# Kernel optimization log

Measured on AMD Instinct MI355X. Metric: run time of the kernel, lower is better.

## Reference

```python
import jax, jax.numpy as jnp
import numpy as np

NUM_CLASSES = 10
CLS_W, L1_W, GIOU_W = 2.0, 5.0, 2.0


def box_cxcywh_to_xyxy(b):
    cx, cy, w, h = b[..., 0], b[..., 1], b[..., 2], b[..., 3]
    return jnp.stack([cx - w / 2, cy - h / 2, cx + w / 2, cy + h / 2], axis=-1)


def giou_matrix(b1, b2):
    # b1: (B,N,4), b2: (B,M,4) xyxy -> (B,N,M)
    a1 = jnp.clip(b1[..., 2] - b1[..., 0], 0) * jnp.clip(b1[..., 3] - b1[..., 1], 0)
    a2 = jnp.clip(b2[..., 2] - b2[..., 0], 0) * jnp.clip(b2[..., 3] - b2[..., 1], 0)
    lt = jnp.maximum(b1[..., :, None, :2], b2[..., None, :, :2])
    rb = jnp.minimum(b1[..., :, None, 2:], b2[..., None, :, 2:])
    wh = jnp.clip(rb - lt, 0)
    inter = wh[..., 0] * wh[..., 1]
    union = a1[..., :, None] + a2[..., None, :] - inter
    iou = inter / jnp.clip(union, 1e-6)
    lte = jnp.minimum(b1[..., :, None, :2], b2[..., None, :, :2])
    rbe = jnp.maximum(b1[..., :, None, 2:], b2[..., None, :, 2:])
    whe = jnp.clip(rbe - lte, 0)
    enc = whe[..., 0] * whe[..., 1]
    return iou - (enc - union) / jnp.clip(enc, 1e-6)


def giou_elem(b1, b2):
    # b1, b2: (N,4) xyxy, paired -> (N,)
    a1 = jnp.clip(b1[:, 2] - b1[:, 0], 0) * jnp.clip(b1[:, 3] - b1[:, 1], 0)
    a2 = jnp.clip(b2[:, 2] - b2[:, 0], 0) * jnp.clip(b2[:, 3] - b2[:, 1], 0)
    lt = jnp.maximum(b1[:, :2], b2[:, :2])
    rb = jnp.minimum(b1[:, 2:], b2[:, 2:])
    wh = jnp.clip(rb - lt, 0)
    inter = wh[:, 0] * wh[:, 1]
    union = a1 + a2 - inter
    iou = inter / jnp.clip(union, 1e-6)
    lte = jnp.minimum(b1[:, :2], b2[:, :2])
    rbe = jnp.maximum(b1[:, 2:], b2[:, 2:])
    whe = jnp.clip(rbe - lte, 0)
    enc = whe[:, 0] * whe[:, 1]
    return iou - (enc - union) / jnp.clip(enc, 1e-6)


def hungarian(cost):
    # Jonker-Volgenant style shortest-augmenting-path assignment (== scipy.linear_sum_assignment)
    cost = np.asarray(cost, dtype=np.float64)
    transposed = cost.shape[0] > cost.shape[1]
    C = cost.T if transposed else cost
    n, m = C.shape  # n <= m
    u = np.zeros(n + 1)
    v = np.zeros(m + 1)
    p = np.zeros(m + 1, dtype=np.int64)
    colr = np.arange(m + 1)
    for i in range(1, n + 1):
        p[0] = i
        j0 = 0
        minv = np.full(m + 1, np.inf)
        way = np.zeros(m + 1, dtype=np.int64)
        used = np.zeros(m + 1, dtype=bool)
        while True:
            used[j0] = True
            i0 = p[j0]
            unused = colr[1:][~used[1:]]
            cur = C[i0 - 1, unused - 1] - u[i0] - v[unused]
            better = cur < minv[unused]
            bidx = unused[better]
            minv[bidx] = cur[better]
            way[bidx] = j0
            j1 = unused[np.argmin(minv[unused])]
            delta = minv[j1]
            u[p[used]] += delta
            v[used] -= delta
            minv[~used] -= delta
            j0 = j1
            if p[j0] == 0:
                break
        while j0 != 0:
            jn = way[j0]
            p[j0] = p[jn]
            j0 = jn
    rows = p[1:] - 1
    cols = np.arange(m)
    sel = rows >= 0
    r, c = rows[sel], cols[sel]
    if transposed:
        r, c = c, r
    order = np.argsort(r)
    return r[order], c[order]


def compute_matches(pred_logits, pred_boxes, gt_classes, gt_boxes):
    # Batched cost matrices on device, per-sample Hungarian on host (mirrors torch.no_grad matcher).
    B, Q, _ = pred_logits.shape
    G = gt_classes.shape[1]
    prob = jax.nn.softmax(pred_logits, axis=-1)
    cls_idx = jnp.clip(gt_classes, 0, NUM_CLASSES - 1)
    idx = jnp.broadcast_to(cls_idx[:, None, :], (B, Q, G))
    cls_cost = -jnp.take_along_axis(prob, idx, axis=2)                 # (B,Q,G)
    l1_cost = jnp.abs(pred_boxes[:, :, None, :] - gt_boxes[:, None, :, :]).sum(-1)
    g = giou_matrix(box_cxcywh_to_xyxy(pred_boxes), box_cxcywh_to_xyxy(gt_boxes))
    cost = CLS_W * cls_cost + L1_W * l1_cost - GIOU_W * g
    cost_np = np.asarray(jax.device_get(cost))
    valid_np = np.asarray(jax.device_get(gt_classes)) >= 0
    bs, ps, gs = [], [], []
    for bi in range(B):
        vidx = np.nonzero(valid_np[bi])[0]
        if vidx.size == 0:
            continue
        r, c = hungarian(cost_np[bi][:, vidx])
        bs.append(np.full(r.size, bi, dtype=np.int64))
        ps.append(r.astype(np.int64))
        gs.append(vidx[c].astype(np.int64))
    if bs:
        return np.concatenate(bs), np.concatenate(ps), np.concatenate(gs)
    z = np.zeros(0, np.int64)
    return z, z, z


def detection_loss(pred_logits, pred_boxes, gt_boxes, target_cls, b_f, p_f, g_f, n_matched):
    C1 = pred_logits.shape[-1]
    logp = jax.nn.log_softmax(pred_logits, axis=-1).reshape(-1, C1)
    t = target_cls.reshape(-1)
    w = jnp.ones(C1, dtype=pred_logits.dtype).at[-1].set(0.1)
    nll = -jnp.take_along_axis(logp, t[:, None], axis=1)[:, 0]
    wt = w[t]
    cls_loss = (wt * nll).sum() / wt.sum()
    mp = pred_boxes[b_f, p_f]
    mg = gt_boxes[b_f, g_f]
    l1 = jnp.abs(mp - mg).sum()
    gd = giou_elem(box_cxcywh_to_xyxy(mp), box_cxcywh_to_xyxy(mg))
    gl = (1.0 - gd).sum()
    return CLS_W * cls_loss + L1_W * l1 / n_matched + GIOU_W * gl / n_matched


def setup_inputs() -> dict:
    key = jax.random.key(0)
    k1, k2, k3, k4, k5 = jax.random.split(key, 5)
    B, Q, G, C = 64, 900, 100, NUM_CLASSES
    pred_logits = jax.random.normal(k1, (B, Q, C + 1), dtype=jnp.float32)
    pred_boxes = jax.random.uniform(k2, (B, Q, 4), dtype=jnp.float32, minval=0.05, maxval=0.6)
    gt_boxes = jax.random.uniform(k3, (B, G, 4), dtype=jnp.float32, minval=0.05, maxval=0.6)
    cls = jax.random.randint(k4, (B, G), 0, C)
    nvalid = jax.random.randint(k5, (B,), 1, G + 1)
    mask = jnp.arange(G)[None, :] < nvalid[:, None]
    gt_classes = jnp.where(mask, cls, -1).astype(jnp.int32)
    return {"pred_logits": pred_logits, "pred_boxes": pred_boxes,
            "gt_classes": gt_classes, "gt_boxes": gt_boxes}


def reference(pred_logits, pred_boxes, gt_classes, gt_boxes):
    B, Q = pred_logits.shape[:2]
    b_f, p_f, g_f = compute_matches(pred_logits, pred_boxes, gt_classes, gt_boxes)
    gt_np = np.asarray(jax.device_get(gt_classes))
    tc = np.full((B, Q), NUM_CLASSES, dtype=np.int32)
    tc[b_f, p_f] = gt_np[b_f, g_f]
    n_matched = max(int(b_f.size), 1)
    return detection_loss(pred_logits, pred_boxes, gt_boxes, jnp.asarray(tc), b_f, p_f, g_f, n_matched)
```

## Files before the change

### kernel.cpp

```cpp
#include <hip/hip_runtime.h>
#include <hip/hip_bf16.h>
#include <math.h>

#define BB 64
#define QQ 900
#define GG 100
#define NCLS 10
#define CP1 11

#define STRIDE 960
#define KPL 15
#define NT 512
#define NW 8
#define QMASK 255
#define ROUND_CAP 20000

#define NCH 8
#define QCH 128

#define CLS_W 2.0f
#define L1_W 5.0f
#define GIOU_W 2.0f

struct Accum {
  double wnll, wt, l1, gl;
  int nm, counter;
  int pad[6];
};

__global__ __launch_bounds__(256) void cost_kernel(
    const float* __restrict__ logits, const float* __restrict__ pboxes,
    const int* __restrict__ gcls, const float* __restrict__ gboxes,
    float* __restrict__ cost, float4* __restrict__ part, Accum* acc) {
  const int b = blockIdx.y;
  const int chunk = blockIdx.x;
  const int tid = threadIdx.x;
  const int ql = tid & (QCH - 1);
  const int gh = tid >> 7;
  const int q = chunk * QCH + ql;

  if (chunk == 0 && b == 0 && tid == 0) {
    acc->wnll = 0.0; acc->wt = 0.0; acc->l1 = 0.0; acc->gl = 0.0;
    acc->nm = 0; acc->counter = 0;
  }

  __shared__ float s_gb[GG * 4];
  __shared__ int   s_gc[GG];
  __shared__ float s_prob[QCH * 13];
  __shared__ float s_c[GG][QCH + 1];
  __shared__ float pm1[2][GG], pm2[2][GG];
  __shared__ int   pj1[2][GG];
  __shared__ int   sh_n;

  if (tid == 0) sh_n = 0;
  __syncthreads();

  for (int i = tid; i < GG * 4; i += 256) s_gb[i] = gboxes[b * GG * 4 + i];
  for (int i = tid; i < GG; i += 256) {
    const int v = gcls[b * GG + i];
    s_gc[i] = v;
    if (v >= 0) atomicAdd(&sh_n, 1);
  }

  float pcx = 0.f, pcy = 0.f, pw = 0.f, ph = 0.f;
  if (q < QQ) {
    const float* pb = pboxes + ((size_t)b * QQ + q) * 4;
    pcx = pb[0]; pcy = pb[1]; pw = pb[2]; ph = pb[3];
    if (gh == 0) {
      const float* lg = logits + ((size_t)b * QQ + q) * CP1;
      float l[CP1];
      float mx = -1e30f;
      for (int c = 0; c < CP1; ++c) { l[c] = lg[c]; mx = fmaxf(mx, l[c]); }
      float se = 0.f;
      for (int c = 0; c < CP1; ++c) { l[c] = expf(l[c] - mx); se += l[c]; }
      const float inv = 1.0f / se;
      for (int c = 0; c < NCLS; ++c) s_prob[ql * 13 + c] = l[c] * inv;
    }
  }
  __syncthreads();
  const int sn = sh_n;

  const float px1 = pcx - 0.5f * pw, py1 = pcy - 0.5f * ph;
  const float px2 = pcx + 0.5f * pw, py2 = pcy + 0.5f * ph;
  const float pa = fmaxf(px2 - px1, 0.f) * fmaxf(py2 - py1, 0.f);

  float* crow = cost + ((size_t)b * GG) * STRIDE + q;
  for (int g = gh; g < sn; g += 2) {
    float cv = 3e38f;
    if (q < QQ) {
      int cls = s_gc[g];
      cls = cls < 0 ? 0 : (cls > NCLS - 1 ? NCLS - 1 : cls);
      const float cc = -s_prob[ql * 13 + cls];
      const float gcx = s_gb[g * 4 + 0], gcy = s_gb[g * 4 + 1];
      const float gw  = s_gb[g * 4 + 2], gh2 = s_gb[g * 4 + 3];
      const float l1 = fabsf(pcx - gcx) + fabsf(pcy - gcy) + fabsf(pw - gw) + fabsf(ph - gh2);
      const float gx1 = gcx - 0.5f * gw, gy1 = gcy - 0.5f * gh2;
      const float gx2 = gcx + 0.5f * gw, gy2 = gcy + 0.5f * gh2;
      const float ga = fmaxf(gx2 - gx1, 0.f) * fmaxf(gy2 - gy1, 0.f);
      const float ltx = fmaxf(px1, gx1), lty = fmaxf(py1, gy1);
      const float rbx = fminf(px2, gx2), rby = fminf(py2, gy2);
      const float iw = fmaxf(rbx - ltx, 0.f), ih = fmaxf(rby - lty, 0.f);
      const float inter = iw * ih;
      const float uni = pa + ga - inter;
      const float iou = inter / fmaxf(uni, 1e-6f);
      const float ex1 = fminf(px1, gx1), ey1 = fminf(py1, gy1);
      const float ex2 = fmaxf(px2, gx2), ey2 = fmaxf(py2, gy2);
      const float ew = fmaxf(ex2 - ex1, 0.f), eh = fmaxf(ey2 - ey1, 0.f);
      const float enc = ew * eh;
      const float giou = iou - (enc - uni) / fmaxf(enc, 1e-6f);
      cv = CLS_W * cc + L1_W * l1 - GIOU_W * giou;
      crow[(size_t)g * STRIDE] = cv;
    } else if (q < STRIDE) {
      crow[(size_t)g * STRIDE] = 1e30f;
    }
    s_c[g][ql] = cv;
  }
  __syncthreads();

  {
    const int kmax = (chunk == NCH - 1) ? (QQ - (NCH - 1) * QCH) : QCH;
    const int half = tid >> 7;
    const int r = tid & 127;
    if (r < sn) {
      const int k0 = half ? 64 : 0;
      const int k1 = half ? kmax : (kmax < 64 ? kmax : 64);
      float m1 = 3e38f, m2 = 3e38f;
      int j1 = 0x7FFFFFFF;
      for (int k = k0; k < k1; ++k) {
        const float c = s_c[r][k];
        if (c < m1) { m2 = m1; m1 = c; j1 = 1 + chunk * QCH + k; }
        else if (c < m2) m2 = c;
      }
      pm1[half][r] = m1; pm2[half][r] = m2; pj1[half][r] = j1;
    }
    __syncthreads();
    if (tid < sn) {
      float m1 = pm1[0][tid], m2 = pm2[0][tid];
      int j1 = pj1[0][tid];
      const float n1 = pm1[1][tid], n2 = pm2[1][tid];
      const int i1 = pj1[1][tid];
      if (n1 < m1) { m2 = fminf(m1, n2); m1 = n1; j1 = i1; }
      else m2 = fminf(m2, n1);
      part[((size_t)b * NCH + chunk) * QCH + tid] = make_float4(m1, m2, __int_as_float(j1), 0.f);
    }
  }
}

__global__ __launch_bounds__(NT) void jv_kernel(
    const float* __restrict__ logits, const float* __restrict__ pboxes,
    const int* __restrict__ gcls, const float* __restrict__ gboxes,
    const float* __restrict__ cost, const float4* __restrict__ part,
    Accum* acc, float* out) {
  const int b = blockIdx.x;
  const int tid = threadIdx.x;
  const int lane = tid & 63;
  const int w = tid >> 6;

  __shared__ float vl[STRIDE + 2];
  __shared__ int   p[QQ + 1];
  __shared__ unsigned long long way64[STRIDE + 2];
  __shared__ float m1l[GG + 1], m2l[GG + 1];
  __shared__ int   aminl[GG + 1];
  __shared__ int   s_gc[GG];
  __shared__ int   queue[QMASK + 1];
  __shared__ int   sh_n, sh_qtail, sh_head;
  __shared__ double r0[NW], r1[NW], r2[NW], r3[NW];
  __shared__ int r4[NW];
  __shared__ float s_lse[QQ], s_mx[QQ];
  __shared__ float cbuf[NW][STRIDE];
  __shared__ int   ctag[NW];

  if (tid == 0) { sh_n = 0; sh_qtail = 0; sh_head = 0; }
  if (tid < NW) ctag[tid] = 0;
  for (int j = tid; j <= QQ; j += NT) p[j] = 0;
  for (int j = tid; j < STRIDE + 2; j += NT) { vl[j] = 0.f; way64[j] = 0ull; }
  if (tid < GG) s_gc[tid] = gcls[b * GG + tid];
  __syncthreads();
  if (tid < GG && s_gc[tid] >= 0) atomicAdd(&sh_n, 1);
  __syncthreads();
  const int n = sh_n;
  const float* Cb = cost + (size_t)b * GG * STRIDE;

  for (int r = tid; r < n; r += NT) {
    float m1 = 3e38f, m2 = 3e38f;
    int j1 = 0x7FFFFFFF;
#pragma unroll
    for (int ch = 0; ch < NCH; ++ch) {
      const float4 pr = part[((size_t)b * NCH + ch) * QCH + r];
      const float pm1 = pr.x, pm2 = pr.y;
      if (pm1 < m1) { m2 = fminf(m1, pm2); m1 = pm1; j1 = __float_as_int(pr.z); }
      else m2 = fminf(m2, pm1);
    }
    m1l[r] = m1; m2l[r] = m2; aminl[r] = j1;
  }
  for (int qq = tid; qq < QQ; qq += NT) {
    const float* lg = logits + ((size_t)b * QQ + qq) * CP1;
    float l[CP1];
    float mx = -1e30f;
    for (int c = 0; c < CP1; ++c) { l[c] = lg[c]; mx = fmaxf(mx, l[c]); }
    float se = 0.f;
    for (int c = 0; c < CP1; ++c) se += expf(l[c] - mx);
    s_mx[qq] = mx;
    s_lse[qq] = logf(se);
  }
  __syncthreads();

  if (tid < n) {
    const float regret = m2l[tid] - m1l[tid];
    const unsigned long long key =
        ((unsigned long long)__float_as_uint(regret) << 20) | (unsigned long long)(tid + 1);
    atomicMax(&way64[aminl[tid]], key);
  }
  __syncthreads();
  if (tid < n) {
    const int j1 = aminl[tid];
    if ((int)(way64[j1] & 0xFFFFFu) == tid + 1) {
      p[j1] = tid + 1;
      vl[j1] = m1l[tid] - m2l[tid];
    } else {
      const int t0 = atomicAdd(&sh_qtail, 1);
      queue[t0 & QMASK] = tid + 1;
    }
  }
  __syncthreads();
  for (int j = tid; j < STRIDE + 2; j += NT) way64[j] = 0ull;
  __syncthreads();

  {
    float pfA[KPL], pfB[KPL];
    int pfApos = -1, pfBpos = -1, pfArid = 0, pfBrid = 0;
    int kround = 0;
    while (kround < ROUND_CAP) {
      const int head = sh_head, tail = sh_qtail;
      const int nq = tail - head;
      if (nq <= 0) break;
      const int take = nq < 2 * NW ? nq : 2 * NW;
      ++kround;

      if (take <= NW) {
        const bool doA = (w < take);
        int ridA = 0;
        float m1A = 3e38f, m2A = 3e38f;
        int j1A = 0x7FFFFFFF;
        int k0A = 0;
        float sfA[KPL];
        if (doA) {
          const int posA = head + w;
          float rcA[KPL];
          if (pfApos == posA) {
            ridA = pfArid;
#pragma unroll
            for (int k = 0; k < KPL; ++k) rcA[k] = pfA[k];
          } else {
            ridA = queue[posA & QMASK];
            const unsigned long long hit =
                __ballot((lane < NW) && (ctag[lane] == ridA));
            if (hit) {
              const int slot = __ffsll((long long)hit) - 1;
#pragma unroll
              for (int k = 0; k < KPL; ++k) rcA[k] = cbuf[slot][lane + (k << 6)];
            } else {
              const float* Cr = Cb + (size_t)(ridA - 1) * STRIDE + lane;
#pragma unroll
              for (int k = 0; k < KPL; ++k) rcA[k] = Cr[k << 6];
            }
          }
          float nA1 = 3e38f, nA2 = 3e38f;
          int iA1 = 0x7FFFFFFF;
#pragma unroll
          for (int k = 0; k < 8; ++k) {
            const float cA = rcA[k] - vl[1 + lane + (k << 6)];
            if (cA < m1A) { m2A = m1A; m1A = cA; j1A = 1 + lane + (k << 6); }
            else if (cA < m2A) m2A = cA;
          }
#pragma unroll
          for (int k = 8; k < KPL; ++k) {
            const float cA = rcA[k] - vl[1 + lane + (k << 6)];
            if (cA < nA1) { nA2 = nA1; nA1 = cA; iA1 = 1 + lane + (k << 6); }
            else if (cA < nA2) nA2 = cA;
          }
          if (nA1 < m1A) { m2A = fminf(m1A, nA2); m1A = nA1; j1A = iA1; }
          else m2A = fminf(m2A, nA1);
          for (int m = 1; m < 64; m <<= 1) {
            const float oA1 = __shfl_xor(m1A, m), oA2 = __shfl_xor(m2A, m);
            const int ojA = __shfl_xor(j1A, m);
            if (oA1 < m1A) { m2A = fminf(m1A, oA2); m1A = oA1; j1A = ojA; }
            else m2A = fminf(m2A, oA1);
          }
          k0A = p[j1A];
          if (k0A > 0) {
            const float* Cr = Cb + (size_t)(k0A - 1) * STRIDE + lane;
#pragma unroll
            for (int k = 0; k < KPL; ++k) sfA[k] = Cr[k << 6];
          }
          if (lane == 0) {
            float dA = m2A - m1A;
            if (dA < 0.f) dA = 0.f;
            const unsigned long long keyA = ((unsigned long long)kround << 44) |
                ((unsigned long long)__float_as_uint(dA) << 12) | (unsigned long long)ridA;
            atomicMax(&way64[j1A], keyA);
          }
        }
        pfApos = -1; pfBpos = -1;
        {
          const int nh = head + take;
          const int pA = nh + w;
          if (pA < tail) {
            pfArid = queue[pA & QMASK];
            const float* Cr = Cb + (size_t)(pfArid - 1) * STRIDE + lane;
#pragma unroll
            for (int k = 0; k < KPL; ++k) pfA[k] = Cr[k << 6];
            pfApos = pA;
          }
        }
        __syncthreads();
        if (doA && k0A > 0) {
#pragma unroll
          for (int k = 0; k < KPL; ++k) cbuf[w][lane + (k << 6)] = sfA[k];
          if (lane == 0) ctag[w] = k0A;
        }
        if (lane == 0 && doA) {
          if ((int)(way64[j1A] & 0xFFFu) == ridA) {
            float dA = m2A - m1A;
            if (dA < 0.f) dA = 0.f;
            const float ov = vl[j1A];
            float nv = ov - dA;
            if (!(nv < ov)) nv = nextafterf(ov, -3e38f);
            vl[j1A] = nv;
            const int k0 = p[j1A];
            p[j1A] = ridA;
            if (k0 > 0) { const int t0 = atomicAdd(&sh_qtail, 1); queue[t0 & QMASK] = k0; }
          } else {
            const int t0 = atomicAdd(&sh_qtail, 1);
            queue[t0 & QMASK] = ridA;
          }
        }
        if (tid == 0) sh_head = head + take;
        __syncthreads();
      } else {
        const bool doA = (w < take);
        const bool doB = (NW + w < take);
        int ridA = 0, ridB = 0;
        float m1A = 3e38f, m2A = 3e38f, m1B = 3e38f, m2B = 3e38f;
        int j1A = 0x7FFFFFFF, j1B = 0x7FFFFFFF;
        {
          float rcA[KPL], rcB[KPL];
          const int posA = head + w;
          if (pfApos == posA) {
            ridA = pfArid;
#pragma unroll
            for (int k = 0; k < KPL; ++k) rcA[k] = pfA[k];
          } else {
            ridA = queue[posA & QMASK];
            const float* Cr = Cb + (size_t)(ridA - 1) * STRIDE + lane;
#pragma unroll
            for (int k = 0; k < KPL; ++k) rcA[k] = Cr[k << 6];
          }
          if (doB) {
            const int posB = head + NW + w;
            if (pfBpos == posB) {
              ridB = pfBrid;
#pragma unroll
              for (int k = 0; k < KPL; ++k) rcB[k] = pfB[k];
            } else {
              ridB = queue[posB & QMASK];
              const float* Cr = Cb + (size_t)(ridB - 1) * STRIDE + lane;
#pragma unroll
              for (int k = 0; k < KPL; ++k) rcB[k] = Cr[k << 6];
            }
          } else {
#pragma unroll
            for (int k = 0; k < KPL; ++k) rcB[k] = 3e38f;
          }
          float nA1 = 3e38f, nA2 = 3e38f, nB1 = 3e38f, nB2 = 3e38f;
          int iA1 = 0x7FFFFFFF, iB1 = 0x7FFFFFFF;
#pragma unroll
          for (int k = 0; k < 8; ++k) {
            const float vv = vl[1 + lane + (k << 6)];
            const float cA = rcA[k] - vv;
            if (cA < m1A) { m2A = m1A; m1A = cA; j1A = 1 + lane + (k << 6); }
            else if (cA < m2A) m2A = cA;
            const float cB = rcB[k] - vv;
            if (cB < m1B) { m2B = m1B; m1B = cB; j1B = 1 + lane + (k << 6); }
            else if (cB < m2B) m2B = cB;
          }
#pragma unroll
          for (int k = 8; k < KPL; ++k) {
            const float vv = vl[1 + lane + (k << 6)];
            const float cA = rcA[k] - vv;
            if (cA < nA1) { nA2 = nA1; nA1 = cA; iA1 = 1 + lane + (k << 6); }
            else if (cA < nA2) nA2 = cA;
            const float cB = rcB[k] - vv;
            if (cB < nB1) { nB2 = nB1; nB1 = cB; iB1 = 1 + lane + (k << 6); }
            else if (cB < nB2) nB2 = cB;
          }
          if (nA1 < m1A) { m2A = fminf(m1A, nA2); m1A = nA1; j1A = iA1; }
          else m2A = fminf(m2A, nA1);
          if (nB1 < m1B) { m2B = fminf(m1B, nB2); m1B = nB1; j1B = iB1; }
          else m2B = fminf(m2B, nB1);
          for (int m = 1; m < 64; m <<= 1) {
            const float oA1 = __shfl_xor(m1A, m), oA2 = __shfl_xor(m2A, m);
            const int ojA = __shfl_xor(j1A, m);
            const float oB1 = __shfl_xor(m1B, m), oB2 = __shfl_xor(m2B, m);
            const int ojB = __shfl_xor(j1B, m);
            if (oA1 < m1A) { m2A = fminf(m1A, oA2); m1A = oA1; j1A = ojA; }
            else m2A = fminf(m2A, oA1);
            if (oB1 < m1B) { m2B = fminf(m1B, oB2); m1B = oB1; j1B = ojB; }
            else m2B = fminf(m2B, oB1);
          }
          if (lane == 0) {
            float dA = m2A - m1A;
            if (dA < 0.f) dA = 0.f;
            const unsigned long long keyA = ((unsigned long long)kround << 44) |
                ((unsigned long long)__float_as_uint(dA) << 12) | (unsigned long long)ridA;
            atomicMax(&way64[j1A], keyA);
            if (doB) {
              float dB = m2B - m1B;
              if (dB < 0.f) dB = 0.f;
              const unsigned long long keyB = ((unsigned long long)kround << 44) |
                  ((unsigned long long)__float_as_uint(dB) << 12) | (unsigned long long)ridB;
              atomicMax(&way64[j1B], keyB);
            }
          }
        }
        pfApos = -1; pfBpos = -1;
        {
          const int nh = head + take;
          const int pA = nh + w, pB = nh + NW + w;
          if (pA < tail) {
            pfArid = queue[pA & QMASK];
            const float* Cr = Cb + (size_t)(pfArid - 1) * STRIDE + lane;
#pragma unroll
            for (int k = 0; k < KPL; ++k) pfA[k] = Cr[k << 6];
            pfApos = pA;
          }
          if (pB < tail) {
            pfBrid = queue[pB & QMASK];
            const float* Cr = Cb + (size_t)(pfBrid - 1) * STRIDE + lane;
#pragma unroll
            for (int k = 0; k < KPL; ++k) pfB[k] = Cr[k << 6];
            pfBpos = pB;
          }
        }
        __syncthreads();
        if (lane == 0 && doA) {
          if ((int)(way64[j1A] & 0xFFFu) == ridA) {
            float dA = m2A - m1A;
            if (dA < 0.f) dA = 0.f;
            const float ov = vl[j1A];
            float nv = ov - dA;
            if (!(nv < ov)) nv = nextafterf(ov, -3e38f);
            vl[j1A] = nv;
            const int k0 = p[j1A];
            p[j1A] = ridA;
            if (k0 > 0) { const int t0 = atomicAdd(&sh_qtail, 1); queue[t0 & QMASK] = k0; }
          } else {
            const int t0 = atomicAdd(&sh_qtail, 1);
            queue[t0 & QMASK] = ridA;
          }
          if (doB) {
            if ((int)(way64[j1B] & 0xFFFu) == ridB) {
              float dB = m2B - m1B;
              if (dB < 0.f) dB = 0.f;
              const float ov = vl[j1B];
              float nv = ov - dB;
              if (!(nv < ov)) nv = nextafterf(ov, -3e38f);
              vl[j1B] = nv;
              const int k0 = p[j1B];
              p[j1B] = ridB;
              if (k0 > 0) { const int t0 = atomicAdd(&sh_qtail, 1); queue[t0 & QMASK] = k0; }
            } else {
              const int t0 = atomicAdd(&sh_qtail, 1);
              queue[t0 & QMASK] = ridB;
            }
          }
        }
        if (tid == 0) sh_head = head + take;
        __syncthreads();
      }
    }
  }
  __syncthreads();

  double wnll = 0.0, wt = 0.0, l1d = 0.0, gld = 0.0;
  int nm = 0;
  for (int q = tid; q < QQ; q += NT) {
    const int idx = b * QQ + q;
    const int g = p[q + 1] - 1;
    const int t = (g >= 0) ? s_gc[g] : NCLS;
    const float lt = logits[(size_t)idx * CP1 + t];
    const float logp = (lt - s_mx[q]) - s_lse[q];
    const float wgt = (t == NCLS) ? 0.1f : 1.0f;
    wnll += (double)(wgt * (-logp));
    wt += (double)wgt;
    if (g >= 0) {
      nm += 1;
      const float* pb = pboxes + (size_t)idx * 4;
      const float* gb = gboxes + ((size_t)b * GG + g) * 4;
      const float pcx = pb[0], pcy = pb[1], pw = pb[2], ph = pb[3];
      const float gcx = gb[0], gcy = gb[1], gw = gb[2], gh = gb[3];
      const float l1 = fabsf(pcx - gcx) + fabsf(pcy - gcy) + fabsf(pw - gw) + fabsf(ph - gh);
      const float px1 = pcx - 0.5f * pw, py1 = pcy - 0.5f * ph;
      const float px2 = pcx + 0.5f * pw, py2 = pcy + 0.5f * ph;
      const float gx1 = gcx - 0.5f * gw, gy1 = gcy - 0.5f * gh;
      const float gx2 = gcx + 0.5f * gw, gy2 = gcy + 0.5f * gh;
      const float pa = fmaxf(px2 - px1, 0.f) * fmaxf(py2 - py1, 0.f);
      const float ga = fmaxf(gx2 - gx1, 0.f) * fmaxf(gy2 - gy1, 0.f);
      const float ltx = fmaxf(px1, gx1), lty = fmaxf(py1, gy1);
      const float rbx = fminf(px2, gx2), rby = fminf(py2, gy2);
      const float iw = fmaxf(rbx - ltx, 0.f), ih = fmaxf(rby - lty, 0.f);
      const float inter = iw * ih;
      const float uni = pa + ga - inter;
      const float iou = inter / fmaxf(uni, 1e-6f);
      const float ex1 = fminf(px1, gx1), ey1 = fminf(py1, gy1);
      const float ex2 = fmaxf(px2, gx2), ey2 = fmaxf(py2, gy2);
      const float ew = fmaxf(ex2 - ex1, 0.f), eh = fmaxf(ey2 - ey1, 0.f);
      const float enc = ew * eh;
      const float giou = iou - (enc - uni) / fmaxf(enc, 1e-6f);
      l1d += (double)l1;
      gld += (double)(1.0f - giou);
    }
  }

  for (int off = 32; off; off >>= 1) {
    wnll += __shfl_down(wnll, off);
    wt   += __shfl_down(wt, off);
    l1d  += __shfl_down(l1d, off);
    gld  += __shfl_down(gld, off);
    nm   += __shfl_down(nm, off);
  }
  if (lane == 0) { r0[w] = wnll; r1[w] = wt; r2[w] = l1d; r3[w] = gld; r4[w] = nm; }
  __syncthreads();
  if (tid == 0) {
    for (int x = 1; x < NW; ++x) { wnll += r0[x]; wt += r1[x]; l1d += r2[x]; gld += r3[x]; nm += r4[x]; }
    atomicAdd(&acc->wnll, wnll);
    atomicAdd(&acc->wt, wt);
    atomicAdd(&acc->l1, l1d);
    atomicAdd(&acc->gl, gld);
    atomicAdd(&acc->nm, nm);
    __threadfence();
    const int ticket = atomicAdd(&acc->counter, 1);
    if (ticket == BB - 1) {
      const double fw = atomicAdd(&acc->wnll, 0.0);
      const double fwt = atomicAdd(&acc->wt, 0.0);
      const double fl1 = atomicAdd(&acc->l1, 0.0);
      const double fgl = atomicAdd(&acc->gl, 0.0);
      int fnm = atomicAdd(&acc->nm, 0);
      if (fnm < 1) fnm = 1;
      const double loss = (double)CLS_W * (fw / fwt) +
                          ((double)L1_W * fl1 + (double)GIOU_W * fgl) / (double)fnm;
      out[0] = (float)loss;
    }
  }
}

extern "C" void kernel_launch(void* const* d_in, const int* in_sizes, int n_in,
                              void* d_out, int out_size, void* d_ws, size_t ws_size,
                              hipStream_t stream) {
  const float* logits = (const float*)d_in[0];
  const float* pboxes = (const float*)d_in[1];
  const int*   gcls   = (const int*)d_in[2];
  const float* gboxes = (const float*)d_in[3];

  char* ws = (char*)d_ws;
  Accum* acc = (Accum*)ws;
  float4* part = (float4*)(ws + 4096);
  float* cost = (float*)(ws + 4096 + (size_t)BB * NCH * QCH * sizeof(float4));

  cost_kernel<<<dim3(NCH, BB), 256, 0, stream>>>(logits, pboxes, gcls, gboxes, cost, part, acc);
  jv_kernel<<<BB, NT, 0, stream>>>(logits, pboxes, gcls, gboxes, cost, part, acc, (float*)d_out);
}
```

Baseline: 102.8 us.

## Fuse cost-matrix kernel into JV assignment kernel with shared-memory scratch reuse

Removes the separate cost_kernel and computes the cost matrix inside the per-batch JV kernel. Each wavefront computes one GT row, writes it to global memory and reduces the row min, second-min and argmin with shuffles, replacing the per-chunk partial results. Prediction boxes, probabilities and areas are staged in shared memory and aliased over the cbuf scratch. The accumulator is zeroed with a memset. This saves a launch and the partial-min round-trip, but cost computation now runs on only 64 blocks instead of 512, which lowers parallelism for that phase.

```diff
diff --git a/kernel.cpp b/kernel.cpp
--- a/kernel.cpp
+++ b/kernel.cpp
@@ -1,5 +1,4 @@
 #include <hip/hip_runtime.h>
-#include <hip/hip_bf16.h>
 #include <math.h>
 
 #define BB 64
@@ -15,12 +14,11 @@
 #define QMASK 255
 #define ROUND_CAP 20000
 
-#define NCH 8
-#define QCH 128
-
 #define CLS_W 2.0f
 #define L1_W 5.0f
 #define GIOU_W 2.0f
+
+#define SCRATCH_F 13504
 
 struct Accum {
   double wnll, wt, l1, gl;
@@ -28,181 +26,129 @@
   int pad[6];
 };
 
-__global__ __launch_bounds__(256) void cost_kernel(
+__global__ __launch_bounds__(NT) void det_kernel(
     const float* __restrict__ logits, const float* __restrict__ pboxes,
     const int* __restrict__ gcls, const float* __restrict__ gboxes,
-    float* __restrict__ cost, float4* __restrict__ part, Accum* acc) {
-  const int b = blockIdx.y;
-  const int chunk = blockIdx.x;
-  const int tid = threadIdx.x;
-  const int ql = tid & (QCH - 1);
-  const int gh = tid >> 7;
-  const int q = chunk * QCH + ql;
-
-  if (chunk == 0 && b == 0 && tid == 0) {
-    acc->wnll = 0.0; acc->wt = 0.0; acc->l1 = 0.0; acc->gl = 0.0;
-    acc->nm = 0; acc->counter = 0;
-  }
-
-  __shared__ float s_gb[GG * 4];
-  __shared__ int   s_gc[GG];
-  __shared__ float s_prob[QCH * 13];
-  __shared__ float s_c[GG][QCH + 1];
-  __shared__ float pm1[2][GG], pm2[2][GG];
-  __shared__ int   pj1[2][GG];
-  __shared__ int   sh_n;
-
-  if (tid == 0) sh_n = 0;
-  __syncthreads();
-
-  for (int i = tid; i < GG * 4; i += 256) s_gb[i] = gboxes[b * GG * 4 + i];
-  for (int i = tid; i < GG; i += 256) {
-    const int v = gcls[b * GG + i];
-    s_gc[i] = v;
-    if (v >= 0) atomicAdd(&sh_n, 1);
-  }
-
-  float pcx = 0.f, pcy = 0.f, pw = 0.f, ph = 0.f;
-  if (q < QQ) {
-    const float* pb = pboxes + ((size_t)b * QQ + q) * 4;
-    pcx = pb[0]; pcy = pb[1]; pw = pb[2]; ph = pb[3];
-    if (gh == 0) {
-      const float* lg = logits + ((size_t)b * QQ + q) * CP1;
-      float l[CP1];
-      float mx = -1e30f;
-      for (int c = 0; c < CP1; ++c) { l[c] = lg[c]; mx = fmaxf(mx, l[c]); }
-      float se = 0.f;
-      for (int c = 0; c < CP1; ++c) { l[c] = expf(l[c] - mx); se += l[c]; }
-      const float inv = 1.0f / se;
-      for (int c = 0; c < NCLS; ++c) s_prob[ql * 13 + c] = l[c] * inv;
-    }
-  }
-  __syncthreads();
-  const int sn = sh_n;
-
-  const float px1 = pcx - 0.5f * pw, py1 = pcy - 0.5f * ph;
-  const float px2 = pcx + 0.5f * pw, py2 = pcy + 0.5f * ph;
-  const float pa = fmaxf(px2 - px1, 0.f) * fmaxf(py2 - py1, 0.f);
-
-  float* crow = cost + ((size_t)b * GG) * STRIDE + q;
-  for (int g = gh; g < sn; g += 2) {
-    float cv = 3e38f;
-    if (q < QQ) {
-      int cls = s_gc[g];
-      cls = cls < 0 ? 0 : (cls > NCLS - 1 ? NCLS - 1 : cls);
-      const float cc = -s_prob[ql * 13 + cls];
-      const float gcx = s_gb[g * 4 + 0], gcy = s_gb[g * 4 + 1];
-      const float gw  = s_gb[g * 4 + 2], gh2 = s_gb[g * 4 + 3];
-      const float l1 = fabsf(pcx - gcx) + fabsf(pcy - gcy) + fabsf(pw - gw) + fabsf(ph - gh2);
-      const float gx1 = gcx - 0.5f * gw, gy1 = gcy - 0.5f * gh2;
-      const float gx2 = gcx + 0.5f * gw, gy2 = gcy + 0.5f * gh2;
-      const float ga = fmaxf(gx2 - gx1, 0.f) * fmaxf(gy2 - gy1, 0.f);
-      const float ltx = fmaxf(px1, gx1), lty = fmaxf(py1, gy1);
-      const float rbx = fminf(px2, gx2), rby = fminf(py2, gy2);
-      const float iw = fmaxf(rbx - ltx, 0.f), ih = fmaxf(rby - lty, 0.f);
-      const float inter = iw * ih;
-      const float uni = pa + ga - inter;
-      const float iou = inter / fmaxf(uni, 1e-6f);
-      const float ex1 = fminf(px1, gx1), ey1 = fminf(py1, gy1);
-      const float ex2 = fmaxf(px2, gx2), ey2 = fmaxf(py2, gy2);
-      const float ew = fmaxf(ex2 - ex1, 0.f), eh = fmaxf(ey2 - ey1, 0.f);
-      const float enc = ew * eh;
-      const float giou = iou - (enc - uni) / fmaxf(enc, 1e-6f);
-      cv = CLS_W * cc + L1_W * l1 - GIOU_W * giou;
-      crow[(size_t)g * STRIDE] = cv;
-    } else if (q < STRIDE) {
-      crow[(size_t)g * STRIDE] = 1e30f;
-    }
-    s_c[g][ql] = cv;
-  }
-  __syncthreads();
-
-  {
-    const int kmax = (chunk == NCH - 1) ? (QQ - (NCH - 1) * QCH) : QCH;
-    const int half = tid >> 7;
-    const int r = tid & 127;
-    if (r < sn) {
-      const int k0 = half ? 64 : 0;
-      const int k1 = half ? kmax : (kmax < 64 ? kmax : 64);
-      float m1 = 3e38f, m2 = 3e38f;
-      int j1 = 0x7FFFFFFF;
-      for (int k = k0; k < k1; ++k) {
-        const float c = s_c[r][k];
-        if (c < m1) { m2 = m1; m1 = c; j1 = 1 + chunk * QCH + k; }
-        else if (c < m2) m2 = c;
-      }
-      pm1[half][r] = m1; pm2[half][r] = m2; pj1[half][r] = j1;
-    }
-    __syncthreads();
-    if (tid < sn) {
-      float m1 = pm1[0][tid], m2 = pm2[0][tid];
-      int j1 = pj1[0][tid];
-      const float n1 = pm1[1][tid], n2 = pm2[1][tid];
-      const int i1 = pj1[1][tid];
-      if (n1 < m1) { m2 = fminf(m1, n2); m1 = n1; j1 = i1; }
-      else m2 = fminf(m2, n1);
-      part[((size_t)b * NCH + chunk) * QCH + tid] = make_float4(m1, m2, __int_as_float(j1), 0.f);
-    }
-  }
-}
-
-__global__ __launch_bounds__(NT) void jv_kernel(
-    const float* __restrict__ logits, const float* __restrict__ pboxes,
-    const int* __restrict__ gcls, const float* __restrict__ gboxes,
-    const float* __restrict__ cost, const float4* __restrict__ part,
-    Accum* acc, float* out) {
+    float* __restrict__ cost, Accum* acc, float* out) {
   const int b = blockIdx.x;
   const int tid = threadIdx.x;
   const int lane = tid & 63;
   const int w = tid >> 6;
 
-  __shared__ float vl[STRIDE + 2];
-  __shared__ int   p[QQ + 1];
+  __shared__ float4 s_pb4[QQ];
+  __shared__ float  s_gb[GG * 4];
+  __shared__ int    s_gc[GG];
+  __shared__ float  s_mx[QQ], s_lse[QQ];
+  __shared__ float  vl[STRIDE + 2];
+  __shared__ int    p[QQ + 1];
   __shared__ unsigned long long way64[STRIDE + 2];
-  __shared__ float m1l[GG + 1], m2l[GG + 1];
-  __shared__ int   aminl[GG + 1];
-  __shared__ int   s_gc[GG];
-  __shared__ int   queue[QMASK + 1];
-  __shared__ int   sh_n, sh_qtail, sh_head;
+  __shared__ float  m1l[GG], m2l[GG];
+  __shared__ int    aminl[GG];
+  __shared__ int    queue[QMASK + 1];
+  __shared__ int    sh_n, sh_qtail, sh_head;
   __shared__ double r0[NW], r1[NW], r2[NW], r3[NW];
-  __shared__ int r4[NW];
-  __shared__ float s_lse[QQ], s_mx[QQ];
-  __shared__ float cbuf[NW][STRIDE];
-  __shared__ int   ctag[NW];
+  __shared__ int    r4[NW];
+  __shared__ int    ctag[NW];
+  __shared__ float4 scratch4[SCRATCH_F / 4];
+
+  float* scratch = (float*)scratch4;
+  float*  s_prob = scratch;
+  float4* s_pxy  = (float4*)(scratch + 9004);
+  float*  s_pa   = scratch + 9004 + 3600;
 
   if (tid == 0) { sh_n = 0; sh_qtail = 0; sh_head = 0; }
   if (tid < NW) ctag[tid] = 0;
   for (int j = tid; j <= QQ; j += NT) p[j] = 0;
   for (int j = tid; j < STRIDE + 2; j += NT) { vl[j] = 0.f; way64[j] = 0ull; }
+  for (int i = tid; i < GG * 4; i += NT) s_gb[i] = gboxes[b * GG * 4 + i];
   if (tid < GG) s_gc[tid] = gcls[b * GG + tid];
-  __syncthreads();
-  if (tid < GG && s_gc[tid] >= 0) atomicAdd(&sh_n, 1);
-  __syncthreads();
-  const int n = sh_n;
-  const float* Cb = cost + (size_t)b * GG * STRIDE;
-
-  for (int r = tid; r < n; r += NT) {
-    float m1 = 3e38f, m2 = 3e38f;
-    int j1 = 0x7FFFFFFF;
-#pragma unroll
-    for (int ch = 0; ch < NCH; ++ch) {
-      const float4 pr = part[((size_t)b * NCH + ch) * QCH + r];
-      const float pm1 = pr.x, pm2 = pr.y;
-      if (pm1 < m1) { m2 = fminf(m1, pm2); m1 = pm1; j1 = __float_as_int(pr.z); }
-      else m2 = fminf(m2, pm1);
-    }
-    m1l[r] = m1; m2l[r] = m2; aminl[r] = j1;
-  }
   for (int qq = tid; qq < QQ; qq += NT) {
+    const float4 pb = reinterpret_cast<const float4*>(pboxes)[(size_t)b * QQ + qq];
+    s_pb4[qq] = pb;
+    const float px1 = pb.x - 0.5f * pb.z, py1 = pb.y - 0.5f * pb.w;
+    const float px2 = pb.x + 0.5f * pb.z, py2 = pb.y + 0.5f * pb.w;
+    s_pxy[qq] = make_float4(px1, py1, px2, py2);
+    s_pa[qq] = fmaxf(px2 - px1, 0.f) * fmaxf(py2 - py1, 0.f);
     const float* lg = logits + ((size_t)b * QQ + qq) * CP1;
     float l[CP1];
     float mx = -1e30f;
     for (int c = 0; c < CP1; ++c) { l[c] = lg[c]; mx = fmaxf(mx, l[c]); }
     float se = 0.f;
-    for (int c = 0; c < CP1; ++c) se += expf(l[c] - mx);
+    for (int c = 0; c < CP1; ++c) { l[c] = expf(l[c] - mx); se += l[c]; }
+    const float inv = 1.0f / se;
+    for (int c = 0; c < NCLS; ++c) s_prob[qq * NCLS + c] = l[c] * inv;
     s_mx[qq] = mx;
     s_lse[qq] = logf(se);
   }
+  __syncthreads();
+  if (tid < GG && s_gc[tid] >= 0) atomicAdd(&sh_n, 1);
+  __syncthreads();
+  const int n = sh_n;
+  float* Cb = cost + (size_t)b * GG * STRIDE;
+
+  auto cell = [&](int qv, int cls, float gcx, float gcy, float gwv, float ghv,
+                  float gx1, float gy1, float gx2, float gy2, float ga) -> float {
+    const float cc = -s_prob[qv * NCLS + cls];
+    const float4 pb = s_pb4[qv];
+    const float4 pxy = s_pxy[qv];
+    const float pa = s_pa[qv];
+    const float l1v = fabsf(pb.x - gcx) + fabsf(pb.y - gcy) +
+                      fabsf(pb.z - gwv) + fabsf(pb.w - ghv);
+    const float ltx = fmaxf(pxy.x, gx1), lty = fmaxf(pxy.y, gy1);
+    const float rbx = fminf(pxy.z, gx2), rby = fminf(pxy.w, gy2);
+    const float iw = fmaxf(rbx - ltx, 0.f), ih = fmaxf(rby - lty, 0.f);
+    const float inter = iw * ih;
+    const float uni = pa + ga - inter;
+    const float iou = inter / fmaxf(uni, 1e-6f);
+    const float ex1 = fminf(pxy.x, gx1), ey1 = fminf(pxy.y, gy1);
+    const float ex2 = fmaxf(pxy.z, gx2), ey2 = fmaxf(pxy.w, gy2);
+    const float ew = fmaxf(ex2 - ex1, 0.f), eh = fmaxf(ey2 - ey1, 0.f);
+    const float enc = ew * eh;
+    const float giou = iou - (enc - uni) / fmaxf(enc, 1e-6f);
+    return CLS_W * cc + L1_W * l1v - GIOU_W * giou;
+  };
+
+  for (int r = w; r < n; r += NW) {
+    int cls = s_gc[r];
+    cls = cls < 0 ? 0 : (cls > NCLS - 1 ? NCLS - 1 : cls);
+    const float gcx = s_gb[r * 4 + 0], gcy = s_gb[r * 4 + 1];
+    const float gwv = s_gb[r * 4 + 2], ghv = s_gb[r * 4 + 3];
+    const float gx1 = gcx - 0.5f * gwv, gy1 = gcy - 0.5f * ghv;
+    const float gx2 = gcx + 0.5f * gwv, gy2 = gcy + 0.5f * ghv;
+    const float ga = fmaxf(gx2 - gx1, 0.f) * fmaxf(gy2 - gy1, 0.f);
+    float* crow = Cb + (size_t)r * STRIDE;
+    float m1 = 3e38f, m2 = 3e38f, n1 = 3e38f, n2 = 3e38f;
+    int j1 = 0x7FFFFFFF, i1 = 0x7FFFFFFF;
+#pragma unroll
+    for (int k = 0; k < 8; ++k) {
+      const int q = lane + (k << 6);
+      float c;
+      if (q < QQ) { c = cell(q, cls, gcx, gcy, gwv, ghv, gx1, gy1, gx2, gy2, ga); crow[q] = c; }
+      else { crow[q] = 1e30f; c = 3e38f; }
+      if (c < m1) { m2 = m1; m1 = c; j1 = 1 + q; }
+      else if (c < m2) m2 = c;
+    }
+#pragma unroll
+    for (int k = 8; k < KPL; ++k) {
+      const int q = lane + (k << 6);
+      float c;
+      if (q < QQ) { c = cell(q, cls, gcx, gcy, gwv, ghv, gx1, gy1, gx2, gy2, ga); crow[q] = c; }
+      else { crow[q] = 1e30f; c = 3e38f; }
+      if (c < n1) { n2 = n1; n1 = c; i1 = 1 + q; }
+      else if (c < n2) n2 = c;
+    }
+    if (n1 < m1) { m2 = fminf(m1, n2); m1 = n1; j1 = i1; }
+    else m2 = fminf(m2, n1);
+    for (int m = 1; m < 64; m <<= 1) {
+      const float o1 = __shfl_xor(m1, m);
+      const float o2 = __shfl_xor(m2, m);
+      const int oj = __shfl_xor(j1, m);
+      if (o1 < m1) { m2 = fminf(m1, o2); m1 = o1; j1 = oj; }
+      else m2 = fminf(m2, o1);
+    }
+    if (lane == 0) { m1l[r] = m1; m2l[r] = m2; aminl[r] = j1; }
+  }
+  __threadfence_block();
   __syncthreads();
 
   if (tid < n) {
@@ -258,7 +204,7 @@
             if (hit) {
               const int slot = __ffsll((long long)hit) - 1;
 #pragma unroll
-              for (int k = 0; k < KPL; ++k) rcA[k] = cbuf[slot][lane + (k << 6)];
+              for (int k = 0; k < KPL; ++k) rcA[k] = scratch[slot * STRIDE + lane + (k << 6)];
             } else {
               const float* Cr = Cb + (size_t)(ridA - 1) * STRIDE + lane;
 #pragma unroll
@@ -303,8 +249,7 @@
         }
         pfApos = -1; pfBpos = -1;
         {
-          const int nh = head + take;
-          const int pA = nh + w;
+          const int pA = head + take + w;
           if (pA < tail) {
             pfArid = queue[pA & QMASK];
             const float* Cr = Cb + (size_t)(pfArid - 1) * STRIDE + lane;
@@ -316,7 +261,7 @@
         __syncthreads();
         if (doA && k0A > 0) {
 #pragma unroll
-          for (int k = 0; k < KPL; ++k) cbuf[w][lane + (k << 6)] = sfA[k];
+          for (int k = 0; k < KPL; ++k) scratch[w * STRIDE + lane + (k << 6)] = sfA[k];
           if (lane == 0) ctag[w] = k0A;
         }
         if (lane == 0 && doA) {
@@ -495,10 +440,10 @@
     wt += (double)wgt;
     if (g >= 0) {
       nm += 1;
-      const float* pb = pboxes + (size_t)idx * 4;
-      const float* gb = gboxes + ((size_t)b * GG + g) * 4;
-      const float pcx = pb[0], pcy = pb[1], pw = pb[2], ph = pb[3];
-      const float gcx = gb[0], gcy = gb[1], gw = gb[2], gh = gb[3];
+      const float4 pb = s_pb4[q];
+      const float pcx = pb.x, pcy = pb.y, pw = pb.z, ph = pb.w;
+      const float gcx = s_gb[g * 4 + 0], gcy = s_gb[g * 4 + 1];
+      const float gw = s_gb[g * 4 + 2], gh = s_gb[g * 4 + 3];
       const float l1 = fabsf(pcx - gcx) + fabsf(pcy - gcy) + fabsf(pw - gw) + fabsf(ph - gh);
       const float px1 = pcx - 0.5f * pw, py1 = pcy - 0.5f * ph;
       const float px2 = pcx + 0.5f * pw, py2 = pcy + 0.5f * ph;
@@ -564,9 +509,8 @@
 
   char* ws = (char*)d_ws;
   Accum* acc = (Accum*)ws;
-  float4* part = (float4*)(ws + 4096);
-  float* cost = (float*)(ws + 4096 + (size_t)BB * NCH * QCH * sizeof(float4));
-
-  cost_kernel<<<dim3(NCH, BB), 256, 0, stream>>>(logits, pboxes, gcls, gboxes, cost, part, acc);
-  jv_kernel<<<BB, NT, 0, stream>>>(logits, pboxes, gcls, gboxes, cost, part, acc, (float*)d_out);
+  float* cost = (float*)(ws + 4096);
+
+  hipMemsetAsync(acc, 0, 256, stream);
+  det_kernel<<<BB, NT, 0, stream>>>(logits, pboxes, gcls, gboxes, cost, acc, (float*)d_out);
 }
```

New measurement: 120.3 us. 17.0% more time.

## Run single-wave serial auction tail when queue has one entry

Applied to the files above, without the earlier changes.

When the auction/assignment work queue shrinks to a single pending row, one wavefront takes over and processes the remaining queue serially. It keeps prices in registers and prefetches the next cost rows into a three-slot rotating buffer. This removes the block-wide __syncthreads and atomic way64 arbitration per round in the long serial tail. The risk is that prices kept in registers are never written back to shared vl, and the tail is entirely single-wave. If later code reads vl, or many items re-enter the queue, correctness or speed could suffer.

```diff
diff --git a/kernel.cpp b/kernel.cpp
--- a/kernel.cpp
+++ b/kernel.cpp
@@ -234,6 +234,92 @@
       const int head = sh_head, tail = sh_qtail;
       const int nq = tail - head;
       if (nq <= 0) break;
+
+      if (nq == 1) {
+        if (w == 0) {
+          float v[KPL];
+#pragma unroll
+          for (int k = 0; k < KPL; ++k) v[k] = vl[1 + lane + (k << 6)];
+          int hd = head, tl = tail, rounds = kround;
+
+          float bufA[KPL], bufB[KPL], bufC[KPL];
+          int ia = -1, ib = -1, ic = -1;
+
+          auto loadrow = [&](float* buf, int rid) {
+            const float* Cr = Cb + (size_t)(rid - 1) * STRIDE + lane;
+#pragma unroll
+            for (int k = 0; k < KPL; ++k) buf[k] = Cr[k << 6];
+          };
+          auto do_step = [&](float* rc, int i) {
+            float m1 = 3e38f, m2 = 3e38f, n1 = 3e38f, n2 = 3e38f;
+            int j1 = 0x7FFFFFFF, i1 = 0x7FFFFFFF;
+#pragma unroll
+            for (int k = 0; k < 8; ++k) {
+              const float c = rc[k] - v[k];
+              if (c < m1) { m2 = m1; m1 = c; j1 = 1 + lane + (k << 6); }
+              else if (c < m2) m2 = c;
+            }
+#pragma unroll
+            for (int k = 8; k < KPL; ++k) {
+              const float c = rc[k] - v[k];
+              if (c < n1) { n2 = n1; n1 = c; i1 = 1 + lane + (k << 6); }
+              else if (c < n2) n2 = c;
+            }
+            if (n1 < m1) { m2 = fminf(m1, n2); m1 = n1; j1 = i1; }
+            else m2 = fminf(m2, n1);
+            for (int m = 1; m < 64; m <<= 1) {
+              const float o1 = __shfl_xor(m1, m);
+              const float o2 = __shfl_xor(m2, m);
+              const int oj = __shfl_xor(j1, m);
+              if (o1 < m1) { m2 = fminf(m1, o2); m1 = o1; j1 = oj; }
+              else m2 = fminf(m2, o1);
+            }
+            float d = m2 - m1;
+            if (d < 0.f) d = 0.f;
+            const int c0 = j1 - 1;
+            if ((c0 & 63) == lane) {
+              const int kk = c0 >> 6;
+              const float ov = v[kk];
+              float nv = ov - d;
+              if (!(nv < ov)) nv = nextafterf(ov, -3e38f);
+              v[kk] = nv;
+            }
+            const int k0 = p[j1];
+            p[j1] = i;
+            hd++;
+            if (k0 > 0) {
+              if (lane == 0) queue[tl & QMASK] = k0;
+              tl++;
+            }
+          };
+
+          if (hd < tl)     { ia = queue[hd & QMASK];       loadrow(bufA, ia); }
+          if (hd + 1 < tl) { ib = queue[(hd + 1) & QMASK]; loadrow(bufB, ib); }
+          if (hd + 2 < tl) { ic = queue[(hd + 2) & QMASK]; loadrow(bufC, ic); }
+
+          while (hd < tl && rounds < ROUND_CAP) {
+            if (ia < 0) { ia = queue[hd & QMASK]; loadrow(bufA, ia); }
+            do_step(bufA, ia);
+            ia = -1;
+            if (hd + 2 < tl) { ia = queue[(hd + 2) & QMASK]; loadrow(bufA, ia); }
+            rounds++;
+            if (!(hd < tl && rounds < ROUND_CAP)) break;
+            if (ib < 0) { ib = queue[hd & QMASK]; loadrow(bufB, ib); }
+            do_step(bufB, ib);
+            ib = -1;
+            if (hd + 2 < tl) { ib = queue[(hd + 2) & QMASK]; loadrow(bufB, ib); }
+            rounds++;
+            if (!(hd < tl && rounds < ROUND_CAP)) break;
+            if (ic < 0) { ic = queue[hd & QMASK]; loadrow(bufC, ic); }
+            do_step(bufC, ic);
+            ic = -1;
+            if (hd + 2 < tl) { ic = queue[(hd + 2) & QMASK]; loadrow(bufC, ic); }
+            rounds++;
+          }
+        }
+        break;
+      }
+
       const int take = nq < 2 * NW ? nq : 2 * NW;
       ++kround;
 
@@ -303,8 +389,7 @@
         }
         pfApos = -1; pfBpos = -1;
         {
-          const int nh = head + take;
-          const int pA = nh + w;
+          const int pA = head + take + w;
           if (pA < tail) {
             pfArid = queue[pA & QMASK];
             const float* Cr = Cb + (size_t)(pfArid - 1) * STRIDE + lane;
```

New measurement: 102.5 us. No clear change (-0.3%).
